# Kernel optimization log

Measured on AMD Instinct MI355X. Metric: run time of the kernel, lower is better.

## Reference

```python
import jax, jax.numpy as jnp
import numpy as np

KERNEL_MUL = 2.0
KERNEL_NUM = 5
FIX_SIGMA = None


def setup_inputs() -> dict:
    key = jax.random.key(0)
    k1, k2 = jax.random.split(key)
    B, N, D = 4, 2048, 64
    return {
        "input": jax.random.normal(k1, (B, N, D), dtype=jnp.float32),
        "target": jax.random.normal(k2, (B, N, D), dtype=jnp.float32),
    }


def _mmd(x, y):
    B = x.shape[0]
    x = x.reshape(B, -1, x.shape[-1])
    y = y.reshape(B, -1, y.shape[-1])
    n = x.shape[1]
    total = jnp.concatenate([x, y], axis=1)          # [B, N, D], N = n + m
    N = total.shape[1]
    # pairwise squared L2 via |a|^2 + |b|^2 - 2 a.b (avoids [B,N,N,D] tensor)
    sq = jnp.sum(total * total, axis=-1)             # [B, N]
    gram = jnp.einsum('bnd,bmd->bnm', total, total)  # [B, N, N]
    L2 = sq[:, :, None] + sq[:, None, :] - 2.0 * gram
    if FIX_SIGMA is not None:
        bandwidth = jnp.full((B,), FIX_SIGMA, dtype=L2.dtype)
    else:
        bandwidth = jnp.sum(jax.lax.stop_gradient(L2), axis=(-1, -2)) / (N * N - N)
    bandwidth = bandwidth / (KERNEL_MUL ** (KERNEL_NUM // 2))   # [B]
    # multi-bandwidth Gaussian kernel sum (small fixed loop over KERNEL_NUM)
    kernels = jnp.zeros_like(L2)
    for i in range(KERNEL_NUM):
        bw_i = bandwidth * (KERNEL_MUL ** i)          # [B]
        kernels = kernels + jnp.exp(-L2 / bw_i[:, None, None])
    XX = kernels[:, :n, :n]
    YY = kernels[:, n:, n:]
    XY = kernels[:, :n, n:]
    YX = kernels[:, n:, :n]
    loss = (XX + YY - XY - YX).reshape(B, -1).mean(axis=-1)  # [B]
    return loss


def reference(input, target):
    return _mmd(input, target)
```

## Files before the change

### kernel.cpp

```cpp
#include <hip/hip_runtime.h>

#define N_TOT 4096
#define N_HALF 2048
#define DIMS 64
#define BATCH 4
#define WGRID 64
#define TRI_PER_BATCH 2080
#define NWG (BATCH * TRI_PER_BATCH)

typedef __attribute__((ext_vector_type(8))) short short8;
typedef __attribute__((ext_vector_type(4))) float f32x4;

#if __has_builtin(__builtin_amdgcn_exp2f)
#define EXP2F(x) __builtin_amdgcn_exp2f(x)
#else
#define EXP2F(x) exp2f(x)
#endif

__device__ __forceinline__ unsigned short f2bf_rne(float f) {
    unsigned int u = __float_as_uint(f);
    unsigned int r = (u + 0x7FFFu + ((u >> 16) & 1u)) >> 16;
    return (unsigned short)r;
}
__device__ __forceinline__ float bf2f(unsigned short h) {
    return __uint_as_float(((unsigned int)h) << 16);
}

__global__ __launch_bounds__(256) void prep_kernel(const float* __restrict__ x,
                                                   const float* __restrict__ y,
                                                   unsigned short* __restrict__ hi,
                                                   unsigned short* __restrict__ lo,
                                                   float* __restrict__ sq,
                                                   float* __restrict__ ssq_part,
                                                   float* __restrict__ colsum_part) {
    int g = blockIdx.x;
    int t = threadIdx.x;
    bool isx = g < 128;
    int gg = isx ? g : g - 128;
    int base = gg << 12;
    int b = gg >> 5;
    const float* src = isx ? x : y;

    float q_acc = 0.f;
    float4 c_acc = {0.f, 0.f, 0.f, 0.f};
#pragma unroll
    for (int it = 0; it < 4; ++it) {
        int e = base + (it << 10) + (t << 2);
        int rem = e & 131071;
        float4 v = *(const float4*)(src + e);
        unsigned dst = (unsigned)b * 262144u + (isx ? 0u : 131072u) + (unsigned)rem;
        ushort4 h, l;
        h.x = f2bf_rne(v.x); l.x = f2bf_rne(v.x - bf2f(h.x));
        h.y = f2bf_rne(v.y); l.y = f2bf_rne(v.y - bf2f(h.y));
        h.z = f2bf_rne(v.z); l.z = f2bf_rne(v.z - bf2f(h.z));
        h.w = f2bf_rne(v.w); l.w = f2bf_rne(v.w - bf2f(h.w));
        *(ushort4*)(hi + dst) = h;
        *(ushort4*)(lo + dst) = l;

        float p = fmaf(v.x, v.x, fmaf(v.y, v.y, fmaf(v.z, v.z, v.w * v.w)));
        p += __shfl_xor(p, 1);
        p += __shfl_xor(p, 2);
        p += __shfl_xor(p, 4);
        p += __shfl_xor(p, 8);
        int rwi = rem >> 6;
        if ((t & 15) == 0)
            sq[b * N_TOT + (isx ? rwi : N_HALF + rwi)] = p;

        float q = p;
        q += __shfl_xor(q, 16);
        q += __shfl_xor(q, 32);
        q_acc += q;

        float4 c = v;
        c.x += __shfl_xor(c.x, 16); c.y += __shfl_xor(c.y, 16);
        c.z += __shfl_xor(c.z, 16); c.w += __shfl_xor(c.w, 16);
        c.x += __shfl_xor(c.x, 32); c.y += __shfl_xor(c.y, 32);
        c.z += __shfl_xor(c.z, 32); c.w += __shfl_xor(c.w, 32);
        c_acc.x += c.x; c_acc.y += c.y; c_acc.z += c.z; c_acc.w += c.w;
    }

    __shared__ float wsum[4];
    __shared__ float4 csh[4][16];
    int wid = t >> 6;
    if ((t & 63) == 0) wsum[wid] = q_acc;
    if ((t & 63) < 16) csh[wid][t & 63] = c_acc;
    __syncthreads();
    if (t == 0) ssq_part[g] = wsum[0] + wsum[1] + wsum[2] + wsum[3];
    if (t < 16) {
        float4 s0 = csh[0][t], s1 = csh[1][t], s2 = csh[2][t], s3 = csh[3][t];
        float4 o;
        o.x = s0.x + s1.x + s2.x + s3.x;
        o.y = s0.y + s1.y + s2.y + s3.y;
        o.z = s0.z + s1.z + s2.z + s3.z;
        o.w = s0.w + s1.w + s2.w + s3.w;
        *(float4*)(colsum_part + (size_t)g * 64 + t * 4) = o;
    }
}

__global__ __launch_bounds__(256) void bw_kernel(const float* __restrict__ ssq_part,
                                                 const float* __restrict__ colsum_part,
                                                 float* __restrict__ k0arr) {
    int b = blockIdx.x;
    int t = threadIdx.x;
    int c = t & 63, q = t >> 6;
    float cs = 0.f;
#pragma unroll
    for (int pp = 0; pp < 16; ++pp) {
        int p = q * 16 + pp;
        int g = (p < 32) ? (b * 32 + p) : (128 + b * 32 + (p - 32));
        cs += colsum_part[(size_t)g * 64 + c];
    }
    __shared__ float csq[4][64];
    csq[q][c] = cs;
    __syncthreads();
    if (t < 64) {
        float col = csq[0][t] + csq[1][t] + csq[2][t] + csq[3][t];
        double cc = (double)col * (double)col;
#pragma unroll
        for (int o = 32; o > 0; o >>= 1) cc += __shfl_xor(cc, o);
        int g = (t < 32) ? (b * 32 + t) : (128 + b * 32 + (t - 32));
        double sd = (double)ssq_part[g];
#pragma unroll
        for (int o = 32; o > 0; o >>= 1) sd += __shfl_xor(sd, o);
        if (t == 0) {
            double sumL2 = 2.0 * (double)N_TOT * sd - 2.0 * cc;
            double bw = sumL2 / ((double)N_TOT * (double)N_TOT - (double)N_TOT);
            bw *= 0.25;
            k0arr[b] = (float)(-1.4426950408889634 / bw);
        }
    }
}

__global__ void mmd_mfma(const unsigned short* __restrict__ hi,
                         const unsigned short* __restrict__ lo,
                         const float* __restrict__ sq,
                         const float* __restrict__ k0arr,
                         double* __restrict__ pblock) {
    int wg0 = blockIdx.x;
    int wg = (wg0 & 7) * (NWG / 8) + (wg0 >> 3);
    int b = wg / TRI_PER_BATCH;
    int r = wg % TRI_PER_BATCH;
    int ib = 0, cum = 0;
    while (r >= cum + (WGRID - ib)) { cum += WGRID - ib; ++ib; }
    int jb = ib + (r - cum);
    unsigned i0 = (unsigned)ib * 64u;
    unsigned j0 = (unsigned)jb * 64u;
    int lane = threadIdx.x;

    const unsigned short* Hb = hi + (unsigned)b * 262144u;
    const unsigned short* Lb = lo + (unsigned)b * 262144u;
    const float* sqb = sq + b * N_TOT;

    __shared__ short ldsB[4096];
    {
        unsigned gb = (j0 + (unsigned)lane) * 64u;
#pragma unroll
        for (int k = 0; k < 8; ++k) {
            short8 v = *(const short8*)(Hb + gb + (unsigned)k * 8u);
            *(short8*)(ldsB + k * 512 + lane * 8) = v;
        }
    }

    bool diag = (ib == jb);
    float wsign = ((i0 < (unsigned)N_HALF) == (j0 < (unsigned)N_HALF)) ? 1.f : -1.f;
    float k16 = k0arr[b] * 0.0625f;
    float m2k16 = -2.f * k16;
    unsigned lrow = (unsigned)(lane & 15);
    unsigned grp = (unsigned)(lane >> 4);
    unsigned rquad = grp * 4u;
    unsigned kbase = grp * 8u;

    float kj16[4];
#pragma unroll
    for (int nf = 0; nf < 4; ++nf)
        kj16[nf] = k16 * sqb[j0 + (unsigned)nf * 16u + lrow];

    const short* B0 = ldsB + grp * 512;
    float eacc0 = 0.f, eacc1 = 0.f;

#pragma unroll
    for (int mf = 0; mf < 4; ++mf) {
        unsigned ra = (i0 + (unsigned)mf * 16u + lrow) * 64u + kbase;
        short8 ah0 = *(const short8*)(Hb + ra);
        short8 ah1 = *(const short8*)(Hb + ra + 32u);
        short8 al0 = *(const short8*)(Lb + ra);
        short8 al1 = *(const short8*)(Lb + ra + 32u);
        float4 sv = *(const float4*)(sqb + i0 + (unsigned)mf * 16u + rquad);
        float ki[4] = {k16 * sv.x, k16 * sv.y, k16 * sv.z, k16 * sv.w};

#pragma unroll
        for (int nf = 0; nf < 4; ++nf) {
            const short* bp = B0 + (nf * 16 + (int)lrow) * 8;
            short8 bh0 = *(const short8*)(bp);
            short8 bh1 = *(const short8*)(bp + 2048);

            f32x4 accP = (f32x4){0.f, 0.f, 0.f, 0.f};
            f32x4 accQ = (f32x4){0.f, 0.f, 0.f, 0.f};
            accP = __builtin_amdgcn_mfma_f32_16x16x32_bf16(ah0, bh0, accP, 0, 0, 0);
            accQ = __builtin_amdgcn_mfma_f32_16x16x32_bf16(ah1, bh1, accQ, 0, 0, 0);
            accP = __builtin_amdgcn_mfma_f32_16x16x32_bf16(al0, bh0, accP, 0, 0, 0);
            accQ = __builtin_amdgcn_mfma_f32_16x16x32_bf16(al1, bh1, accQ, 0, 0, 0);

#pragma unroll
            for (int rg = 0; rg < 4; ++rg) {
                float t16 = fmaf(m2k16, accQ[rg],
                                 fmaf(m2k16, accP[rg], ki[rg] + kj16[nf]));
                float e4 = EXP2F(t16);
                float e3 = e4 * e4;
                float e2 = e3 * e3;
                float e1 = e2 * e2;
                float e0 = e1 * e1;
                float es = ((e0 + e1) + (e2 + e3)) + e4;
                if (diag) {
                    int i = mf * 16 + (int)rquad + rg;
                    int j = nf * 16 + (int)lrow;
                    float w = (j > i) ? 2.f : ((j == i) ? 1.f : 0.f);
                    es *= w;
                }
                if (rg & 1) eacc1 += es; else eacc0 += es;
            }
        }
    }

    double acc_d = (double)((eacc0 + eacc1) * (diag ? wsign : 2.f * wsign));
#pragma unroll
    for (int o = 32; o > 0; o >>= 1) acc_d += __shfl_down(acc_d, o);
    if (lane == 0) pblock[wg] = acc_d;
}

__global__ __launch_bounds__(256) void finalize_kernel(const double* __restrict__ pblock,
                                                       float* __restrict__ out) {
    int b = blockIdx.x, t = threadIdx.x;
    const double* p = pblock + (size_t)b * TRI_PER_BATCH;
    double s = 0.0;
    for (int i = t; i < TRI_PER_BATCH; i += 256) s += p[i];
#pragma unroll
    for (int o = 32; o > 0; o >>= 1) s += __shfl_down(s, o);
    __shared__ double w[4];
    if ((t & 63) == 0) w[t >> 6] = s;
    __syncthreads();
    if (t == 0)
        out[b] = (float)((w[0] + w[1] + w[2] + w[3]) / ((double)N_HALF * (double)N_HALF));
}

extern "C" void kernel_launch(void* const* d_in, const int* in_sizes, int n_in,
                              void* d_out, int out_size, void* d_ws, size_t ws_size,
                              hipStream_t stream) {
    const float* x = (const float*)d_in[0];
    const float* y = (const float*)d_in[1];
    float* out = (float*)d_out;
    char* ws = (char*)d_ws;

    float*  k0arr       = (float*)ws;
    float*  ssq_part    = (float*)(ws + 4096);
    float*  colsum_part = (float*)(ws + 8192);
    double* pblock      = (double*)(ws + 8192);
    float*  sq          = (float*)(ws + 77824);
    unsigned short* tot_hi = (unsigned short*)(ws + 143360);
    unsigned short* tot_lo = (unsigned short*)(ws + 143360 + 2097152);

    prep_kernel<<<256, 256, 0, stream>>>(x, y, tot_hi, tot_lo, sq, ssq_part, colsum_part);
    bw_kernel<<<BATCH, 256, 0, stream>>>(ssq_part, colsum_part, k0arr);
    mmd_mfma<<<NWG, 64, 0, stream>>>(tot_hi, tot_lo, sq, k0arr, pblock);
    finalize_kernel<<<BATCH, 256, 0, stream>>>(pblock, out);
}
```

Before: 43.83 us.

## Widen prep grid, template diagonal tile path, raise wave priority in MMD kernel

The prep kernel now launches 1024 blocks, each converting one float4 per thread instead of looping four times, to expose more parallelism. The bandwidth kernel and workspace layout are adjusted so it can reduce the larger set of partial sums. The main MFMA loop moves into a template on DIAG so that off-diagonal tiles carry no per-element mask, and it is wrapped in s_setprio to raise wave priority. The cost is more partial-sum traffic for the bandwidth reduction and larger workspace offsets.

New measurement: 50.74 us. 15.8% more time.

```diff
diff --git a/kernel.cpp b/kernel.cpp
--- a/kernel.cpp
+++ b/kernel.cpp
@@ -35,55 +35,46 @@
                                                    float* __restrict__ colsum_part) {
     int g = blockIdx.x;
     int t = threadIdx.x;
-    bool isx = g < 128;
-    int gg = isx ? g : g - 128;
-    int base = gg << 12;
-    int b = gg >> 5;
-    const float* src = isx ? x : y;
-
-    float q_acc = 0.f;
-    float4 c_acc = {0.f, 0.f, 0.f, 0.f};
-#pragma unroll
-    for (int it = 0; it < 4; ++it) {
-        int e = base + (it << 10) + (t << 2);
-        int rem = e & 131071;
-        float4 v = *(const float4*)(src + e);
-        unsigned dst = (unsigned)b * 262144u + (isx ? 0u : 131072u) + (unsigned)rem;
-        ushort4 h, l;
-        h.x = f2bf_rne(v.x); l.x = f2bf_rne(v.x - bf2f(h.x));
-        h.y = f2bf_rne(v.y); l.y = f2bf_rne(v.y - bf2f(h.y));
-        h.z = f2bf_rne(v.z); l.z = f2bf_rne(v.z - bf2f(h.z));
-        h.w = f2bf_rne(v.w); l.w = f2bf_rne(v.w - bf2f(h.w));
-        *(ushort4*)(hi + dst) = h;
-        *(ushort4*)(lo + dst) = l;
-
-        float p = fmaf(v.x, v.x, fmaf(v.y, v.y, fmaf(v.z, v.z, v.w * v.w)));
-        p += __shfl_xor(p, 1);
-        p += __shfl_xor(p, 2);
-        p += __shfl_xor(p, 4);
-        p += __shfl_xor(p, 8);
-        int rwi = rem >> 6;
-        if ((t & 15) == 0)
-            sq[b * N_TOT + (isx ? rwi : N_HALF + rwi)] = p;
-
-        float q = p;
-        q += __shfl_xor(q, 16);
-        q += __shfl_xor(q, 32);
-        q_acc += q;
-
-        float4 c = v;
-        c.x += __shfl_xor(c.x, 16); c.y += __shfl_xor(c.y, 16);
-        c.z += __shfl_xor(c.z, 16); c.w += __shfl_xor(c.w, 16);
-        c.x += __shfl_xor(c.x, 32); c.y += __shfl_xor(c.y, 32);
-        c.z += __shfl_xor(c.z, 32); c.w += __shfl_xor(c.w, 32);
-        c_acc.x += c.x; c_acc.y += c.y; c_acc.z += c.z; c_acc.w += c.w;
-    }
-
+    bool isx = g < 512;
+    int gg = isx ? g : g - 512;
+    int e = (gg << 10) + (t << 2);
+    int b = e >> 17;
+    int rem = e & 131071;
+    const float* src = (isx ? x : y) + e;
+    unsigned dst = (unsigned)b * 262144u + (isx ? 0u : 131072u) + (unsigned)rem;
+
+    float4 v = *(const float4*)src;
+    ushort4 h, l;
+    h.x = f2bf_rne(v.x); l.x = f2bf_rne(v.x - bf2f(h.x));
+    h.y = f2bf_rne(v.y); l.y = f2bf_rne(v.y - bf2f(h.y));
+    h.z = f2bf_rne(v.z); l.z = f2bf_rne(v.z - bf2f(h.z));
+    h.w = f2bf_rne(v.w); l.w = f2bf_rne(v.w - bf2f(h.w));
+    *(ushort4*)(hi + dst) = h;
+    *(ushort4*)(lo + dst) = l;
+
+    float p = fmaf(v.x, v.x, fmaf(v.y, v.y, fmaf(v.z, v.z, v.w * v.w)));
+    p += __shfl_xor(p, 1);
+    p += __shfl_xor(p, 2);
+    p += __shfl_xor(p, 4);
+    p += __shfl_xor(p, 8);
+    int rwi = rem >> 6;
+    if ((t & 15) == 0)
+        sq[b * N_TOT + (isx ? rwi : N_HALF + rwi)] = p;
+
+    float q = p;
+    q += __shfl_xor(q, 16);
+    q += __shfl_xor(q, 32);
     __shared__ float wsum[4];
+    int wid = t >> 6;
+    if ((t & 63) == 0) wsum[wid] = q;
+
+    float4 c = v;
+    c.x += __shfl_xor(c.x, 16); c.y += __shfl_xor(c.y, 16);
+    c.z += __shfl_xor(c.z, 16); c.w += __shfl_xor(c.w, 16);
+    c.x += __shfl_xor(c.x, 32); c.y += __shfl_xor(c.y, 32);
+    c.z += __shfl_xor(c.z, 32); c.w += __shfl_xor(c.w, 32);
     __shared__ float4 csh[4][16];
-    int wid = t >> 6;
-    if ((t & 63) == 0) wsum[wid] = q_acc;
-    if ((t & 63) < 16) csh[wid][t & 63] = c_acc;
+    if ((t & 63) < 16) csh[wid][t & 63] = c;
     __syncthreads();
     if (t == 0) ssq_part[g] = wsum[0] + wsum[1] + wsum[2] + wsum[3];
     if (t < 16) {
@@ -103,32 +94,96 @@
     int b = blockIdx.x;
     int t = threadIdx.x;
     int c = t & 63, q = t >> 6;
+
     float cs = 0.f;
-#pragma unroll
-    for (int pp = 0; pp < 16; ++pp) {
-        int p = q * 16 + pp;
-        int g = (p < 32) ? (b * 32 + p) : (128 + b * 32 + (p - 32));
+#pragma unroll 8
+    for (int pp = 0; pp < 64; ++pp) {
+        int p = q * 64 + pp;
+        int g = (p < 128) ? (b * 128 + p) : (512 + b * 128 + (p - 128));
         cs += colsum_part[(size_t)g * 64 + c];
     }
     __shared__ float csq[4][64];
     csq[q][c] = cs;
-    __syncthreads();
-    if (t < 64) {
-        float col = csq[0][t] + csq[1][t] + csq[2][t] + csq[3][t];
-        double cc = (double)col * (double)col;
-#pragma unroll
-        for (int o = 32; o > 0; o >>= 1) cc += __shfl_xor(cc, o);
-        int g = (t < 32) ? (b * 32 + t) : (128 + b * 32 + (t - 32));
-        double sd = (double)ssq_part[g];
-#pragma unroll
-        for (int o = 32; o > 0; o >>= 1) sd += __shfl_xor(sd, o);
-        if (t == 0) {
-            double sumL2 = 2.0 * (double)N_TOT * sd - 2.0 * cc;
-            double bw = sumL2 / ((double)N_TOT * (double)N_TOT - (double)N_TOT);
-            bw *= 0.25;
-            k0arr[b] = (float)(-1.4426950408889634 / bw);
+
+    {
+        int p = t;
+        int g = (p < 128) ? (b * 128 + p) : (512 + b * 128 + (p - 128));
+        float sp = ssq_part[g];
+#pragma unroll
+        for (int o = 32; o > 0; o >>= 1) sp += __shfl_xor(sp, o);
+        __shared__ float ssh[4];
+        if ((t & 63) == 0) ssh[q] = sp;
+        __syncthreads();
+        if (t < 64) {
+            float col = csq[0][t] + csq[1][t] + csq[2][t] + csq[3][t];
+            double cc = (double)col * (double)col;
+#pragma unroll
+            for (int o = 32; o > 0; o >>= 1) cc += __shfl_xor(cc, o);
+            if (t == 0) {
+                double sd = (double)ssh[0] + (double)ssh[1] +
+                            (double)ssh[2] + (double)ssh[3];
+                double sumL2 = 2.0 * (double)N_TOT * sd - 2.0 * cc;
+                double bw = sumL2 / ((double)N_TOT * (double)N_TOT - (double)N_TOT);
+                bw *= 0.25;
+                k0arr[b] = (float)(-1.4426950408889634 / bw);
+            }
         }
     }
+}
+
+template <bool DIAG>
+__device__ __forceinline__ float mmd_tile(const unsigned short* __restrict__ Hb,
+                                          const unsigned short* __restrict__ Lb,
+                                          const float* __restrict__ sqb,
+                                          const short* __restrict__ B0,
+                                          unsigned i0, unsigned lrow, unsigned rquad,
+                                          unsigned kbase, float k16, float m2k16,
+                                          const float* __restrict__ kj16) {
+    float eacc0 = 0.f, eacc1 = 0.f;
+#pragma unroll
+    for (int mf = 0; mf < 4; ++mf) {
+        unsigned ra = (i0 + (unsigned)mf * 16u + lrow) * 64u + kbase;
+        short8 ah0 = *(const short8*)(Hb + ra);
+        short8 ah1 = *(const short8*)(Hb + ra + 32u);
+        short8 al0 = *(const short8*)(Lb + ra);
+        short8 al1 = *(const short8*)(Lb + ra + 32u);
+        float4 sv = *(const float4*)(sqb + i0 + (unsigned)mf * 16u + rquad);
+        float ki[4] = {k16 * sv.x, k16 * sv.y, k16 * sv.z, k16 * sv.w};
+
+#pragma unroll
+        for (int nf = 0; nf < 4; ++nf) {
+            const short* bp = B0 + (nf * 16 + (int)lrow) * 8;
+            short8 bh0 = *(const short8*)(bp);
+            short8 bh1 = *(const short8*)(bp + 2048);
+
+            f32x4 accP = (f32x4){0.f, 0.f, 0.f, 0.f};
+            f32x4 accQ = (f32x4){0.f, 0.f, 0.f, 0.f};
+            accP = __builtin_amdgcn_mfma_f32_16x16x32_bf16(ah0, bh0, accP, 0, 0, 0);
+            accQ = __builtin_amdgcn_mfma_f32_16x16x32_bf16(ah1, bh1, accQ, 0, 0, 0);
+            accP = __builtin_amdgcn_mfma_f32_16x16x32_bf16(al0, bh0, accP, 0, 0, 0);
+            accQ = __builtin_amdgcn_mfma_f32_16x16x32_bf16(al1, bh1, accQ, 0, 0, 0);
+
+#pragma unroll
+            for (int rg = 0; rg < 4; ++rg) {
+                float t16 = fmaf(m2k16, accQ[rg],
+                                 fmaf(m2k16, accP[rg], ki[rg] + kj16[nf]));
+                float e4 = EXP2F(t16);
+                float e3 = e4 * e4;
+                float e2 = e3 * e3;
+                float e1 = e2 * e2;
+                float e0 = e1 * e1;
+                float es = ((e0 + e1) + (e2 + e3)) + e4;
+                if constexpr (DIAG) {
+                    int i = mf * 16 + (int)rquad + rg;
+                    int j = nf * 16 + (int)lrow;
+                    float w = (j > i) ? 2.f : ((j == i) ? 1.f : 0.f);
+                    es *= w;
+                }
+                if (rg & 1) eacc1 += es; else eacc0 += es;
+            }
+        }
+    }
+    return eacc0 + eacc1;
 }
 
 __global__ void mmd_mfma(const unsigned short* __restrict__ hi,
@@ -176,53 +231,14 @@
         kj16[nf] = k16 * sqb[j0 + (unsigned)nf * 16u + lrow];
 
     const short* B0 = ldsB + grp * 512;
-    float eacc0 = 0.f, eacc1 = 0.f;
-
-#pragma unroll
-    for (int mf = 0; mf < 4; ++mf) {
-        unsigned ra = (i0 + (unsigned)mf * 16u + lrow) * 64u + kbase;
-        short8 ah0 = *(const short8*)(Hb + ra);
-        short8 ah1 = *(const short8*)(Hb + ra + 32u);
-        short8 al0 = *(const short8*)(Lb + ra);
-        short8 al1 = *(const short8*)(Lb + ra + 32u);
-        float4 sv = *(const float4*)(sqb + i0 + (unsigned)mf * 16u + rquad);
-        float ki[4] = {k16 * sv.x, k16 * sv.y, k16 * sv.z, k16 * sv.w};
-
-#pragma unroll
-        for (int nf = 0; nf < 4; ++nf) {
-            const short* bp = B0 + (nf * 16 + (int)lrow) * 8;
-            short8 bh0 = *(const short8*)(bp);
-            short8 bh1 = *(const short8*)(bp + 2048);
-
-            f32x4 accP = (f32x4){0.f, 0.f, 0.f, 0.f};
-            f32x4 accQ = (f32x4){0.f, 0.f, 0.f, 0.f};
-            accP = __builtin_amdgcn_mfma_f32_16x16x32_bf16(ah0, bh0, accP, 0, 0, 0);
-            accQ = __builtin_amdgcn_mfma_f32_16x16x32_bf16(ah1, bh1, accQ, 0, 0, 0);
-            accP = __builtin_amdgcn_mfma_f32_16x16x32_bf16(al0, bh0, accP, 0, 0, 0);
-            accQ = __builtin_amdgcn_mfma_f32_16x16x32_bf16(al1, bh1, accQ, 0, 0, 0);
-
-#pragma unroll
-            for (int rg = 0; rg < 4; ++rg) {
-                float t16 = fmaf(m2k16, accQ[rg],
-                                 fmaf(m2k16, accP[rg], ki[rg] + kj16[nf]));
-                float e4 = EXP2F(t16);
-                float e3 = e4 * e4;
-                float e2 = e3 * e3;
-                float e1 = e2 * e2;
-                float e0 = e1 * e1;
-                float es = ((e0 + e1) + (e2 + e3)) + e4;
-                if (diag) {
-                    int i = mf * 16 + (int)rquad + rg;
-                    int j = nf * 16 + (int)lrow;
-                    float w = (j > i) ? 2.f : ((j == i) ? 1.f : 0.f);
-                    es *= w;
-                }
-                if (rg & 1) eacc1 += es; else eacc0 += es;
-            }
-        }
-    }
-
-    double acc_d = (double)((eacc0 + eacc1) * (diag ? wsign : 2.f * wsign));
+
+    __builtin_amdgcn_s_setprio(1);
+    float eacc = diag
+        ? mmd_tile<true>(Hb, Lb, sqb, B0, i0, lrow, rquad, kbase, k16, m2k16, kj16)
+        : mmd_tile<false>(Hb, Lb, sqb, B0, i0, lrow, rquad, kbase, k16, m2k16, kj16);
+    __builtin_amdgcn_s_setprio(0);
+
+    double acc_d = (double)(eacc * (diag ? wsign : 2.f * wsign));
 #pragma unroll
     for (int o = 32; o > 0; o >>= 1) acc_d += __shfl_down(acc_d, o);
     if (lane == 0) pblock[wg] = acc_d;
@@ -253,13 +269,13 @@
 
     float*  k0arr       = (float*)ws;
     float*  ssq_part    = (float*)(ws + 4096);
-    float*  colsum_part = (float*)(ws + 8192);
-    double* pblock      = (double*)(ws + 8192);
-    float*  sq          = (float*)(ws + 77824);
-    unsigned short* tot_hi = (unsigned short*)(ws + 143360);
-    unsigned short* tot_lo = (unsigned short*)(ws + 143360 + 2097152);
-
-    prep_kernel<<<256, 256, 0, stream>>>(x, y, tot_hi, tot_lo, sq, ssq_part, colsum_part);
+    float*  colsum_part = (float*)(ws + 12288);
+    double* pblock      = (double*)(ws + 12288);
+    float*  sq          = (float*)(ws + 278528);
+    unsigned short* tot_hi = (unsigned short*)(ws + 344064);
+    unsigned short* tot_lo = (unsigned short*)(ws + 344064 + 2097152);
+
+    prep_kernel<<<1024, 256, 0, stream>>>(x, y, tot_hi, tot_lo, sq, ssq_part, colsum_part);
     bw_kernel<<<BATCH, 256, 0, stream>>>(ssq_part, colsum_part, k0arr);
     mmd_mfma<<<NWG, 64, 0, stream>>>(tot_hi, tot_lo, sq, k0arr, pblock);
     finalize_kernel<<<BATCH, 256, 0, stream>>>(pblock, out);
```
